# Kernel tuning notes

Measured on AMD Instinct MI355X. Metric: run time of the kernel, lower is better.

## Reference

```python
import jax, jax.numpy as jnp
import numpy as np

WINDOW_SIZE = 11
WINDOW_SIGMA = 1.5
LOSS_WEIGHT = 1.0
PAD = WINDOW_SIZE // 2  # 5; applied to BOTH H and W as in the torch source


def _gaussian_window(channels):
    # Matches torch gaussian_window: 1-D gaussian reshaped to (1,1,1,ws),
    # repeated per channel -> OIHW kernel of shape (C, 1, 1, ws).
    coords = np.arange(WINDOW_SIZE, dtype=np.float32) - (WINDOW_SIZE // 2)
    g = np.exp(-coords ** 2 / (2.0 * WINDOW_SIGMA ** 2))
    g = g / g.sum()
    w = np.tile(g.reshape(1, 1, 1, WINDOW_SIZE), (channels, 1, 1, 1))
    return jnp.asarray(w)


def _dwconv(x, w, channels):
    # Depthwise conv, kernel (1, ws), zero padding 5 on both H and W
    # (faithful to F.conv2d(..., padding=5) with a (1,11) kernel, which
    # grows H by 10 -- intentional reproduction of the source behavior).
    return jax.lax.conv_general_dilated(
        x, w,
        window_strides=(1, 1),
        padding=((PAD, PAD), (PAD, PAD)),
        dimension_numbers=('NCHW', 'OIHW', 'NCHW'),
        feature_group_count=channels,
    )


def setup_inputs() -> dict:
    key = jax.random.key(0)
    k1, k2 = jax.random.split(key)
    shape = (16, 3, 512, 512)
    pred = jax.random.uniform(k1, shape, dtype=jnp.float32)
    target = jax.random.uniform(k2, shape, dtype=jnp.float32)
    return {"pred": pred, "target": target}


def reference(pred, target):
    channels = pred.shape[1]
    w = _gaussian_window(channels)
    conv = lambda x: _dwconv(x, w, channels)

    mu1 = conv(pred)              # (B, C, H+10, W)
    mu2 = conv(target)
    mu1_sq = mu1 * mu1
    mu2_sq = mu2 * mu2
    mu1_mu2 = mu1 * mu2

    sigma1_sq = conv(pred * pred) - mu1_sq
    sigma2_sq = conv(target * target) - mu2_sq
    sigma12 = conv(pred * target) - mu1_mu2

    C1 = 0.01 ** 2
    C2 = 0.03 ** 2
    ssim_map = ((2.0 * mu1_mu2 + C1) * (2.0 * sigma12 + C2)) / (
        (mu1_sq + mu2_sq + C1) * (sigma1_sq + sigma2_sq + C2))

    return LOSS_WEIGHT * (1.0 - ssim_map.mean())
```

## Files before the change

kernel.cpp:

```cpp
#include <hip/hip_runtime.h>
#include <hip/hip_fp16.h>
#include <cmath>

#define WS 11

struct GaussHalf {
    unsigned gA[WS];
    unsigned gS[WS];
    unsigned c11, c22;
};

__global__ __launch_bounds__(256, 8) void ssim_row_kernel(
    const float* __restrict__ pred, const float* __restrict__ targ,
    GaussHalf gh, float* __restrict__ partials)
{
    const int t = threadIdx.x;
    const int lane = t & 63;
    const int wid = (blockIdx.x << 2) | (t >> 6);

    const long long off = (long long)wid * 512 + 8 * lane;
    const float* prow = pred + off;
    const float* trow = targ + off;

    const float4 P0 = *reinterpret_cast<const float4*>(prow);
    const float4 P1 = *reinterpret_cast<const float4*>(prow + 4);
    const float4 Q0 = *reinterpret_cast<const float4*>(trow);
    const float4 Q1 = *reinterpret_cast<const float4*>(trow + 4);

    const __half2 pm = __halves2half2(__float2half(1.f), __float2half(-1.f));
    const __half2 C11 = __builtin_bit_cast(__half2, gh.c11);
    const __half2 C22 = __builtin_bit_cast(__half2, gh.c22);

    __half2 w[18];
    {
        const float pv[8] = {P0.x, P0.y, P0.z, P0.w, P1.x, P1.y, P1.z, P1.w};
        const float qv[8] = {Q0.x, Q0.y, Q0.z, Q0.w, Q1.x, Q1.y, Q1.z, Q1.w};
        #pragma unroll
        for (int i = 0; i < 8; ++i)
            w[5 + i] = __floats2half2_rn(pv[i] + qv[i], pv[i] - qv[i]);
    }
    #pragma unroll
    for (int i = 0; i < 5; ++i) {
        const unsigned lu =
            __shfl_up(__builtin_bit_cast(unsigned, w[8 + i]), 1);
        const unsigned ru =
            __shfl_down(__builtin_bit_cast(unsigned, w[5 + i]), 1);
        w[i]      = __builtin_bit_cast(__half2, (lane == 0)  ? 0u : lu);
        w[13 + i] = __builtin_bit_cast(__half2, (lane == 63) ? 0u : ru);
    }
    __half2 s[18];
    #pragma unroll
    for (int i = 0; i < 18; ++i) s[i] = __hmul2(w[i], w[i]);

    float acc = 0.f;
    #pragma unroll
    for (int px = 0; px < 8; ++px) {
        __half2 AB  = __builtin_bit_cast(__half2, 0u);
        __half2 SUV = __builtin_bit_cast(__half2, 0u);
        #pragma unroll
        for (int k = 0; k < WS; ++k) {
            AB  = __hfma2(__builtin_bit_cast(__half2, gh.gA[k]),
                          w[px + k], AB);
            SUV = __hfma2(__builtin_bit_cast(__half2, gh.gS[k]),
                          s[px + k], SUV);
        }
        const __half2 ab2  = __hmul2(AB, AB);
        const __half2 t2d2 = __hfma2(__lowhigh2highlow(ab2), pm, ab2);
        const __half2 tsds = __hfma2(__lowhigh2highlow(SUV), pm, SUV);
        const __half2 dn1  = __hfma2(t2d2, pm, C11);
        const __half2 dl   = __hsub2(tsds, t2d2);
        const __half2 dn2  = __hfma2(dl, pm, C22);
        const __half2 nd   = __hmul2(dn1, dn2);
        const float dd = __half2float(__low2half(nd));
        const float nn = __half2float(__high2half(nd));
        acc = fmaf(nn, __builtin_amdgcn_rcpf(dd), acc);
    }

    #pragma unroll
    for (int offr = 32; offr > 0; offr >>= 1)
        acc += __shfl_down(acc, offr);
    if (lane == 0)
        partials[wid] = acc;
}

__global__ __launch_bounds__(1024) void ssim_final_kernel(
    const float* __restrict__ partials, float* __restrict__ out)
{
    const int t = threadIdx.x;
    double d = 0.0;
    #pragma unroll
    for (int i = 0; i < 24; ++i)
        d += (double)partials[t + 1024 * i];
    #pragma unroll
    for (int offr = 32; offr > 0; offr >>= 1)
        d += __shfl_down(d, offr);
    __shared__ double wsumd[16];
    const int lane = t & 63, wave = t >> 6;
    if (lane == 0) wsumd[wave] = d;
    __syncthreads();
    if (t == 0) {
        double s = 245760.0;
        #pragma unroll
        for (int i = 0; i < 16; ++i) s += wsumd[i];
        out[0] = (float)(1.0 - s / 12828672.0);
    }
}

static unsigned packh2(float x) {
    const __half h = __float2half(x);
    unsigned short hb;
    __builtin_memcpy(&hb, &h, 2);
    return ((unsigned)hb << 16) | hb;
}

extern "C" void kernel_launch(void* const* d_in, const int* in_sizes, int n_in,
                              void* d_out, int out_size, void* d_ws, size_t ws_size,
                              hipStream_t stream) {
    const float* pred = (const float*)d_in[0];
    const float* targ = (const float*)d_in[1];
    float* out = (float*)d_out;
    float* partials = (float*)d_ws;

    GaussHalf gh;
    double graw[WS], s = 0.0;
    for (int i = 0; i < WS; ++i) {
        const double c = (double)(i - WS / 2);
        graw[i] = exp(-c * c / (2.0 * 1.5 * 1.5));
        s += graw[i];
    }
    for (int i = 0; i < WS; ++i) {
        const double g = graw[i] / s;
        gh.gA[i] = packh2((float)(g * 0.70710678118654752));
        gh.gS[i] = packh2((float)(g * 0.5));
    }
    gh.c11 = packh2(0.0001f);
    gh.c22 = packh2(0.0009f);

    ssim_row_kernel<<<6144, 256, 0, stream>>>(pred, targ, gh, partials);
    ssim_final_kernel<<<1, 1024, 0, stream>>>(partials, out);
}
```

Baseline: 24.89 us.

## Load row halos via bounds-checked buffer loads instead of wave shuffles

Each lane now fetches its 5-element left and right halo directly from global memory using raw buffer_load instructions. A per-row buffer descriptor sized to 2048 bytes makes out-of-range reads return zero, which supplies the convolution padding for free. This removes the 10 cross-lane shuffles and their lane-boundary selects. The cost is extra redundant loads per lane, mostly cache hits. Blocks also shrink to 128 threads with twice as many blocks and a different occupancy hint.

```diff
diff --git a/kernel.cpp b/kernel.cpp
--- a/kernel.cpp
+++ b/kernel.cpp
@@ -3,6 +3,8 @@
 #include <cmath>
 
 #define WS 11
+
+typedef unsigned int u32x4_t __attribute__((ext_vector_type(4)));
 
 struct GaussHalf {
     unsigned gA[WS];
@@ -10,47 +12,79 @@
     unsigned c11, c22;
 };
 
-__global__ __launch_bounds__(256, 8) void ssim_row_kernel(
+__device__ __forceinline__ u32x4_t make_row_srsrc(const float* p) {
+    const unsigned long long a = (unsigned long long)p;
+    u32x4_t r;
+    r.x = (unsigned)a;
+    r.y = (unsigned)(a >> 32);
+    r.z = 2048u;
+    r.w = 0x00020000u;
+    return r;
+}
+__device__ __forceinline__ float4 bl_x4(u32x4_t srd, int voff) {
+    float4 d;
+    asm volatile("buffer_load_dwordx4 %0, %1, %2, 0 offen"
+                 : "=v"(d) : "v"(voff), "s"(srd));
+    return d;
+}
+__device__ __forceinline__ float bl_x1(u32x4_t srd, int voff) {
+    float d;
+    asm volatile("buffer_load_dword %0, %1, %2, 0 offen"
+                 : "=v"(d) : "v"(voff), "s"(srd));
+    return d;
+}
+
+__global__ __launch_bounds__(128, 6) void ssim_row_kernel(
     const float* __restrict__ pred, const float* __restrict__ targ,
     GaussHalf gh, float* __restrict__ partials)
 {
     const int t = threadIdx.x;
     const int lane = t & 63;
-    const int wid = (blockIdx.x << 2) | (t >> 6);
+    const int wid = __builtin_amdgcn_readfirstlane((blockIdx.x << 1) | (t >> 6));
 
-    const long long off = (long long)wid * 512 + 8 * lane;
-    const float* prow = pred + off;
-    const float* trow = targ + off;
+    const int l8 = 8 * lane;
+    const int vL1 = 4 * (l8 - 5);
+    const int vL4 = 4 * (l8 - 4);
+    const int vA  = 4 * l8;
+    const int vB  = 4 * (l8 + 4);
+    const int vR4 = 4 * (l8 + 8);
+    const int vR1 = 4 * (l8 + 12);
 
-    const float4 P0 = *reinterpret_cast<const float4*>(prow);
-    const float4 P1 = *reinterpret_cast<const float4*>(prow + 4);
-    const float4 Q0 = *reinterpret_cast<const float4*>(trow);
-    const float4 Q1 = *reinterpret_cast<const float4*>(trow + 4);
+    const u32x4_t sp = make_row_srsrc(pred + (long long)wid * 512);
+    const u32x4_t sq = make_row_srsrc(targ + (long long)wid * 512);
+
+    const float  pL1 = bl_x1(sp, vL1);
+    const float4 pL4 = bl_x4(sp, vL4);
+    const float4 pA  = bl_x4(sp, vA);
+    const float4 pB  = bl_x4(sp, vB);
+    const float4 pR4 = bl_x4(sp, vR4);
+    const float  pR1 = bl_x1(sp, vR1);
+    const float  qL1 = bl_x1(sq, vL1);
+    const float4 qL4 = bl_x4(sq, vL4);
+    const float4 qA  = bl_x4(sq, vA);
+    const float4 qB  = bl_x4(sq, vB);
+    const float4 qR4 = bl_x4(sq, vR4);
+    const float  qR1 = bl_x1(sq, vR1);
+    asm volatile("s_waitcnt vmcnt(0)" ::: "memory");
+    __builtin_amdgcn_sched_barrier(0);
+
+    const float pv[18] = {pL1, pL4.x, pL4.y, pL4.z, pL4.w,
+                          pA.x, pA.y, pA.z, pA.w, pB.x, pB.y, pB.z, pB.w,
+                          pR4.x, pR4.y, pR4.z, pR4.w, pR1};
+    const float qv[18] = {qL1, qL4.x, qL4.y, qL4.z, qL4.w,
+                          qA.x, qA.y, qA.z, qA.w, qB.x, qB.y, qB.z, qB.w,
+                          qR4.x, qR4.y, qR4.z, qR4.w, qR1};
 
     const __half2 pm = __halves2half2(__float2half(1.f), __float2half(-1.f));
     const __half2 C11 = __builtin_bit_cast(__half2, gh.c11);
     const __half2 C22 = __builtin_bit_cast(__half2, gh.c22);
 
-    __half2 w[18];
-    {
-        const float pv[8] = {P0.x, P0.y, P0.z, P0.w, P1.x, P1.y, P1.z, P1.w};
-        const float qv[8] = {Q0.x, Q0.y, Q0.z, Q0.w, Q1.x, Q1.y, Q1.z, Q1.w};
-        #pragma unroll
-        for (int i = 0; i < 8; ++i)
-            w[5 + i] = __floats2half2_rn(pv[i] + qv[i], pv[i] - qv[i]);
+    __half2 w[18], s[18];
+    #pragma unroll
+    for (int i = 0; i < 18; ++i) {
+        w[i] = __floats2half2_rn(pv[i] + qv[i], pv[i] - qv[i]);
+        s[i] = __hmul2(w[i], w[i]);
     }
-    #pragma unroll
-    for (int i = 0; i < 5; ++i) {
-        const unsigned lu =
-            __shfl_up(__builtin_bit_cast(unsigned, w[8 + i]), 1);
-        const unsigned ru =
-            __shfl_down(__builtin_bit_cast(unsigned, w[5 + i]), 1);
-        w[i]      = __builtin_bit_cast(__half2, (lane == 0)  ? 0u : lu);
-        w[13 + i] = __builtin_bit_cast(__half2, (lane == 63) ? 0u : ru);
-    }
-    __half2 s[18];
-    #pragma unroll
-    for (int i = 0; i < 18; ++i) s[i] = __hmul2(w[i], w[i]);
 
     float acc = 0.f;
     #pragma unroll
@@ -136,6 +170,6 @@
     gh.c11 = packh2(0.0001f);
     gh.c22 = packh2(0.0009f);
 
-    ssim_row_kernel<<<6144, 256, 0, stream>>>(pred, targ, gh, partials);
+    ssim_row_kernel<<<12288, 128, 0, stream>>>(pred, targ, gh, partials);
     ssim_final_kernel<<<1, 1024, 0, stream>>>(partials, out);
 }
```

New measurement: 26.58 us. 6.8% more time.
